# Kernel tuning notes

Measured on AMD Instinct MI355X. Metric: run time of the kernel, lower is better.

## Reference

```python
import jax, jax.numpy as jnp
import numpy as np

B, S, HID = 2, 1024, 4096
H, KV, D = 32, 8, 128
EPS = 1e-6
ROPE_THETA = 1000000.0


def _make_freqs_cis(seq_len, head_dim, theta):
    inv_freq = 1.0 / (theta ** (jnp.arange(0, head_dim, 2, dtype=jnp.float32) / head_dim))
    ang = jnp.arange(seq_len, dtype=jnp.float32)[:, None] * inv_freq[None, :]  # [S, D/2]
    emb = jnp.concatenate([ang, ang], axis=-1)                                 # [S, D]
    cos, sin = jnp.cos(emb), jnp.sin(emb)
    return jnp.stack([cos, sin, -sin], axis=0)                                 # [3, S, D]


def setup_inputs() -> dict:
    key = jax.random.key(0)
    ks = jax.random.split(key, 8)
    scale = 0.02
    return {
        "hidden_states": jax.random.normal(ks[0], (B, S, HID), dtype=jnp.float32),
        "freqs_cis": _make_freqs_cis(S, D, ROPE_THETA),
        "Wq": jax.random.normal(ks[1], (H * D, HID), dtype=jnp.float32) * scale,
        "Wk": jax.random.normal(ks[2], (KV * D, HID), dtype=jnp.float32) * scale,
        "Wv": jax.random.normal(ks[3], (KV * D, HID), dtype=jnp.float32) * scale,
        "Wo": jax.random.normal(ks[4], (HID, H * D), dtype=jnp.float32) * scale,
        "q_norm_w": jnp.ones((D,), jnp.float32) + jax.random.normal(ks[5], (D,), jnp.float32) * scale,
        "k_norm_w": jnp.ones((D,), jnp.float32) + jax.random.normal(ks[6], (D,), jnp.float32) * scale,
    }


def _rmsnorm(x, w):
    # per-head RMSNorm over last dim (rms_norm_add=False -> plain weight multiply)
    return x * jax.lax.rsqrt(jnp.mean(x * x, axis=-1, keepdims=True) + EPS) * w


def _rope(x, cos, sin, nsin):
    # matches apply_rope: e = x*cos; e[:half] += x[half:]*nsin; e[half:] += x[:half]*sin
    half = x.shape[-1] // 2
    e = x * cos
    lo = e[..., :half] + x[..., half:] * nsin[..., :half]
    hi = e[..., half:] + x[..., :half] * sin[..., half:]
    return jnp.concatenate([lo, hi], axis=-1)


def reference(hidden_states, freqs_cis, Wq, Wk, Wv, Wo, q_norm_w, k_norm_w):
    b, s, _ = hidden_states.shape
    # QKV projections (no bias)
    q = jnp.einsum("bsh,oh->bso", hidden_states, Wq).reshape(b, s, H, D).transpose(0, 2, 1, 3)
    k = jnp.einsum("bsh,oh->bso", hidden_states, Wk).reshape(b, s, KV, D).transpose(0, 2, 1, 3)
    v = jnp.einsum("bsh,oh->bso", hidden_states, Wv).reshape(b, s, KV, D).transpose(0, 2, 1, 3)
    # per-head RMSNorm (Qwen3 'gemma3' q/k norms)
    q = _rmsnorm(q, q_norm_w)
    k = _rmsnorm(k, k_norm_w)
    # RoPE
    cos, sin, nsin = freqs_cis[0], freqs_cis[1], freqs_cis[2]  # [S, D] each, broadcast over (b, heads)
    q = _rope(q, cos, sin, nsin)
    k = _rope(k, cos, sin, nsin)
    # GQA: repeat kv heads to match query heads (repeat_interleave dim=1)
    rep = H // KV
    k = jnp.repeat(k, rep, axis=1)
    v = jnp.repeat(v, rep, axis=1)
    # SDPA (no mask, past_key_value=None path)
    scale = D ** -0.5
    attn = jax.nn.softmax(jnp.einsum("bhqd,bhkd->bhqk", q, k) * scale, axis=-1)
    out = jnp.einsum("bhqk,bhkd->bhqd", attn, v)
    out = out.transpose(0, 2, 1, 3).reshape(b, s, H * D)
    return jnp.einsum("bsi,hi->bsh", out, Wo)
```

## Files before the change

### kernel.cpp

```cpp
#include <hip/hip_runtime.h>


typedef __attribute__((ext_vector_type(8))) short s8v;
typedef __attribute__((ext_vector_type(4))) float f4v;
typedef __attribute__((ext_vector_type(8))) unsigned short u8v;
typedef __attribute__((ext_vector_type(4))) float float4v;
typedef __attribute__((ext_vector_type(2))) float float2v;
typedef unsigned short us;

#define SB() __builtin_amdgcn_sched_barrier(0)

__device__ __forceinline__ void BARRIER() {
  asm volatile("" ::: "memory");
  __builtin_amdgcn_s_barrier();
  asm volatile("" ::: "memory");
}

__device__ __forceinline__ us f2b(float f) {
  unsigned u = __builtin_bit_cast(unsigned, f);
  u += 0x7fffu + ((u >> 16) & 1u);
  return (us)(u >> 16);
}
__device__ __forceinline__ float b2f(us h) {
  return __builtin_bit_cast(float, (unsigned)h << 16);
}

__device__ __forceinline__ void gload16(const void* g, void* l) {
  __builtin_amdgcn_global_load_lds(
      (const __attribute__((address_space(1))) unsigned int*)g,
      (__attribute__((address_space(3))) unsigned int*)l, 16, 0, 0);
}

__global__ __launch_bounds__(256) void cvt_all_k(const float* __restrict__ h,
                                                 const float* __restrict__ wq,
                                                 const float* __restrict__ wk,
                                                 const float* __restrict__ wv,
                                                 us* __restrict__ dst) {
  long blk = blockIdx.x;
  const float* src;
  long off;
  if (blk < 4096)        { src = h;  off = 0; }
  else if (blk < 12288)  { src = wq; off = 4096; }
  else if (blk < 14336)  { src = wk; off = 12288; }
  else                   { src = wv; off = 14336; }
  long i = (blk - off) * 2048 + (long)threadIdx.x * 8;
  long o = blk * 2048 + (long)threadIdx.x * 8;
  float4v a = *(const float4v*)(src + i);
  float4v b = *(const float4v*)(src + i + 4);
  u8v v;
  v[0] = f2b(a[0]); v[1] = f2b(a[1]); v[2] = f2b(a[2]); v[3] = f2b(a[3]);
  v[4] = f2b(b[0]); v[5] = f2b(b[1]); v[6] = f2b(b[2]); v[7] = f2b(b[3]);
  *(u8v*)(dst + o) = v;
}

template <int AH, bool F32OUT, bool CVTTAIL>
__global__ __launch_bounds__(512, 2) void gemm8p(const us* __restrict__ A,
                                                 const us* __restrict__ W,
                                                 void* __restrict__ Cv,
                                                 int K, int nkt, int ldc,
                                                 int cm, int cn, int ncn,
                                                 int nGemm,
                                                 const float* __restrict__ csrc,
                                                 us* __restrict__ cdst) {
  if constexpr (CVTTAIL) {
    if ((int)blockIdx.x >= nGemm) {
      long c = (long)((int)blockIdx.x - nGemm) * 512 + threadIdx.x;
      for (; c < 2097152; c += 64 * 512) {
        long i = c * 8;
        float4v x = *(const float4v*)(csrc + i);
        float4v y = *(const float4v*)(csrc + i + 4);
        u8v v;
        v[0] = f2b(x[0]); v[1] = f2b(x[1]); v[2] = f2b(x[2]); v[3] = f2b(x[3]);
        v[4] = f2b(y[0]); v[5] = f2b(y[1]); v[6] = f2b(y[2]); v[7] = f2b(y[3]);
        *(u8v*)(cdst + i) = v;
      }
      return;
    }
  }

  constexpr int FR = AH / 32;
  constexpr int LA = AH / 64;
  constexpr int VM = 2 * LA + 2;

  __shared__ __align__(16) us Ah[2][2][AH * 64];
  __shared__ __align__(16) us Bh[2][2][128 * 64];
  const int tid = threadIdx.x, lane = tid & 63, w = tid >> 6;
  const int wr = w >> 2, wc = w & 3;
  const int lr = lane & 15, lg = lane >> 4;

  const int xcd = (int)blockIdx.x & 7;
  const int i2 = (int)blockIdx.x >> 3;
  const int im = i2 % cm, itn = i2 / cm;
  const long m0 = (long)((xcd / ncn) * cm + im) * (2 * AH);
  const long n0 = (long)((xcd % ncn) * cn + itn) * 256;

  const int rA0 = tid >> 3;
  const int sc0 = ((tid & 7) ^ (rA0 & 7)) << 3;

#define STGH(dst, src, LOADS)                                           \
  do {                                                                  \
    const us* _s = (src);                                               \
    us* _d = (dst);                                                     \
    _Pragma("unroll") for (int l = 0; l < (LOADS); ++l)                 \
      gload16(_s + (long)(rA0 + l * 64) * K + sc0, _d + (l * 512 + tid) * 8); \
  } while (0)

  const us* Asrc = A + m0 * K;
  const us* Bsrc = W + n0 * K;
  const long hKA = (long)AH * K;
  const long hKB = (long)128 * K;

  const int ra = wr * (AH / 2) + lr, rb = wc * 32 + lr;
  const int offA0 = ra * 64 + ((lg ^ (ra & 7)) << 3);
  const int offA1 = ra * 64 + (((4 + lg) ^ (ra & 7)) << 3);
  const int offB0 = rb * 64 + ((lg ^ (rb & 7)) << 3);
  const int offB1 = rb * 64 + (((4 + lg) ^ (rb & 7)) << 3);

  f4v acc[2 * FR][4];
#pragma unroll
  for (int i = 0; i < 2 * FR; ++i)
#pragma unroll
    for (int j = 0; j < 4; ++j) acc[i][j] = (f4v){0.f, 0.f, 0.f, 0.f};

  const int nk = nkt;

  STGH(Ah[0][0], Asrc, LA);
  STGH(Bh[0][0], Bsrc, 2);
  STGH(Bh[0][1], Bsrc + hKB, 2);
  STGH(Ah[0][1], Asrc + hKA, LA);
  STGH(Ah[1][0], Asrc + 64, LA);
  STGH(Bh[1][1], Bsrc + hKB + 64, 2);
  STGH(Ah[1][1], Asrc + hKA + 64, LA);
  asm volatile("s_waitcnt vmcnt(%0)" :: "i"(VM) : "memory");
  BARRIER();

  s8v a[FR][2], b0[2][2], b1[2][2];

#define RD_A(H)                                                         \
  _Pragma("unroll") for (int f = 0; f < FR; ++f) {                      \
    a[f][0] = *(const s8v*)(&Ah[d][H][offA0 + f * 1024]);               \
    a[f][1] = *(const s8v*)(&Ah[d][H][offA1 + f * 1024]);               \
  }
#define RD_B(BB, H)                                                     \
  _Pragma("unroll") for (int g = 0; g < 2; ++g) {                       \
    BB[g][0] = *(const s8v*)(&Bh[d][H][offB0 + g * 1024]);              \
    BB[g][1] = *(const s8v*)(&Bh[d][H][offB1 + g * 1024]);              \
  }
#define QUAD(QM, QN, BB)                                                \
  __builtin_amdgcn_s_setprio(1);                                        \
  _Pragma("unroll") for (int f = 0; f < FR; ++f)                        \
  _Pragma("unroll") for (int g = 0; g < 2; ++g) {                       \
    f4v t = acc[QM * FR + f][QN * 2 + g];                               \
    t = __builtin_amdgcn_mfma_f32_16x16x32_bf16(a[f][0], BB[g][0], t, 0, 0, 0); \
    t = __builtin_amdgcn_mfma_f32_16x16x32_bf16(a[f][1], BB[g][1], t, 0, 0, 0); \
    acc[QM * FR + f][QN * 2 + g] = t;                                   \
  }                                                                     \
  __builtin_amdgcn_s_setprio(0);
#define PREMFMA()                                                       \
  BARRIER();                                                            \
  asm volatile("s_waitcnt lgkmcnt(0)" ::: "memory");                    \
  SB();

  for (int kt = 0; kt < nk; ++kt) {
    const int d = kt & 1;
    const long kb2 = (long)(kt + 2) * 64;
    const bool p1 = (kt + 1 < nk), p2 = (kt + 2 < nk);

    RD_A(0)
    RD_B(b0, 0)
    if (p1) STGH(Bh[d ^ 1][0], Bsrc + (long)(kt + 1) * 64, 2);
    PREMFMA()
    QUAD(0, 0, b0)
    BARRIER();

    RD_B(b1, 1)
    if (p2) STGH(Ah[d][0], Asrc + kb2, LA);
    PREMFMA()
    QUAD(0, 1, b1)
    BARRIER();

    RD_A(1)
    if (p2) STGH(Bh[d][1], Bsrc + hKB + kb2, 2);
    PREMFMA()
    QUAD(1, 1, b1)
    BARRIER();

    if (p2) STGH(Ah[d][1], Asrc + hKA + kb2, LA);
    PREMFMA()
    QUAD(1, 0, b0)
    if (p2) asm volatile("s_waitcnt vmcnt(%0)" :: "i"(VM) : "memory");
    else    asm volatile("s_waitcnt vmcnt(0)" ::: "memory");
    BARRIER();
  }

#pragma unroll
  for (int qm = 0; qm < 2; ++qm)
#pragma unroll
    for (int f = 0; f < FR; ++f) {
      long row = m0 + qm * AH + wr * (AH / 2) + f * 16 + lg * 4;
#pragma unroll
      for (int qn = 0; qn < 2; ++qn)
#pragma unroll
        for (int g = 0; g < 2; ++g) {
          long col = n0 + qn * 128 + wc * 32 + g * 16 + lr;
          f4v v = acc[qm * FR + f][qn * 2 + g];
          if constexpr (F32OUT) {
            float* C = (float*)Cv;
#pragma unroll
            for (int r = 0; r < 4; ++r) C[(row + r) * ldc + col] = v[r];
          } else {
            us* C = (us*)Cv;
#pragma unroll
            for (int r = 0; r < 4; ++r) C[(row + r) * ldc + col] = f2b(v[r]);
          }
        }
    }
#undef STGH
#undef RD_A
#undef RD_B
#undef QUAD
#undef PREMFMA
}

__global__ __launch_bounds__(256, 2) void gemm2p128(const us* __restrict__ A,
                                                    const us* __restrict__ W,
                                                    float* __restrict__ C) {
  constexpr int K = 4096, nk = 64, ldc = 4096;
  __shared__ __align__(16) us Ab[2][128 * 64];
  __shared__ __align__(16) us Bb[2][128 * 64];
  const int tid = threadIdx.x, lane = tid & 63, w = tid >> 6;
  const int wm = w & 1, wn = w >> 1;
  const int lr = lane & 15, lg = lane >> 4;

  const int xcd = (int)blockIdx.x & 7;
  const int i2 = (int)blockIdx.x >> 3;
  const long m0 = (long)(i2 & 15) * 128;
  const long n0 = (long)(xcd * 4 + (i2 >> 4)) * 128;

  const int rA0 = tid >> 3;
  const int sc0 = ((tid & 7) ^ (rA0 & 7)) << 3;

  const us* Asrc = A + m0 * K;
  const us* Bsrc = W + n0 * K;

#define STG1(Sb, buf, src)                                               \
  do {                                                                   \
    const us* _s = (src);                                                \
    _Pragma("unroll") for (int l = 0; l < 4; ++l)                        \
      gload16(_s + (long)(rA0 + l * 32) * K + sc0,                       \
              &Sb[buf][(l * 256 + tid) * 8]);                            \
  } while (0)

  const int ra = wm * 64 + lr;
  const int rb = wn * 64 + lr;
  const int offA0 = ra * 64 + ((lg ^ (ra & 7)) << 3);
  const int offA1 = ra * 64 + (((4 + lg) ^ (ra & 7)) << 3);
  const int offB0 = rb * 64 + ((lg ^ (rb & 7)) << 3);
  const int offB1 = rb * 64 + (((4 + lg) ^ (rb & 7)) << 3);

  f4v acc[4][4];
#pragma unroll
  for (int f = 0; f < 4; ++f)
#pragma unroll
    for (int g = 0; g < 4; ++g) acc[f][g] = (f4v){0.f, 0.f, 0.f, 0.f};

  STG1(Ab, 0, Asrc);
  STG1(Bb, 0, Bsrc);
  STG1(Ab, 1, Asrc + 64);
  asm volatile("s_waitcnt vmcnt(4)" ::: "memory");
  BARRIER();

  for (int kt = 0; kt < nk; ++kt) {
    const int d = kt & 1;
    const bool p1 = (kt + 1 < nk), p2 = (kt + 2 < nk);

    s8v a[4][2], b[4][2];
#pragma unroll
    for (int f = 0; f < 4; ++f) {
      a[f][0] = *(const s8v*)(&Ab[d][offA0 + f * 1024]);
      a[f][1] = *(const s8v*)(&Ab[d][offA1 + f * 1024]);
    }
#pragma unroll
    for (int g = 0; g < 4; ++g) {
      b[g][0] = *(const s8v*)(&Bb[d][offB0 + g * 1024]);
      b[g][1] = *(const s8v*)(&Bb[d][offB1 + g * 1024]);
    }
    if (p1) STG1(Bb, d ^ 1, Bsrc + (long)(kt + 1) * 64);
    asm volatile("s_waitcnt lgkmcnt(0)" ::: "memory");
    BARRIER();
    if (p2) STG1(Ab, d, Asrc + (long)(kt + 2) * 64);

    __builtin_amdgcn_s_setprio(1);
#pragma unroll
    for (int f = 0; f < 4; ++f)
#pragma unroll
      for (int g = 0; g < 4; ++g) {
        f4v t = acc[f][g];
        t = __builtin_amdgcn_mfma_f32_16x16x32_bf16(a[f][0], b[g][0], t, 0, 0, 0);
        t = __builtin_amdgcn_mfma_f32_16x16x32_bf16(a[f][1], b[g][1], t, 0, 0, 0);
        acc[f][g] = t;
      }
    __builtin_amdgcn_s_setprio(0);

    if (p2) asm volatile("s_waitcnt vmcnt(4)" ::: "memory");
    else    asm volatile("s_waitcnt vmcnt(0)" ::: "memory");
    BARRIER();
  }

#pragma unroll
  for (int f = 0; f < 4; ++f) {
    long row = m0 + wm * 64 + f * 16 + lg * 4;
#pragma unroll
    for (int g = 0; g < 4; ++g) {
      long col = n0 + wn * 64 + g * 16 + lr;
      f4v v = acc[f][g];
#pragma unroll
      for (int r = 0; r < 4; ++r) C[(row + r) * ldc + col] = v[r];
    }
  }
#undef STG1
}

__global__ __launch_bounds__(256) void rms_rope_k(us* __restrict__ qkv,
                                                  const float* __restrict__ fc,
                                                  const float* __restrict__ kw) {
  int idx = blockIdx.x * 4 + (threadIdx.x >> 6);
  int lane = threadIdx.x & 63;
  int head = idx & 7;
  int row = idx >> 3;
  int s = row & 1023;
  us* p = qkv + (long)row * 6144 + 4096 + head * 128;

  unsigned v = ((const unsigned*)p)[lane];
  float x0 = b2f((us)(v & 0xffff)), x1 = b2f((us)(v >> 16));
  float ss = x0 * x0 + x1 * x1;
#pragma unroll
  for (int off = 32; off; off >>= 1) ss += __shfl_xor(ss, off);
  float r = rsqrtf(ss * (1.0f / 128.0f) + 1e-6f);
  float2v wv = ((const float2v*)kw)[lane];
  float y0 = x0 * r * wv[0], y1 = x1 * r * wv[1];
  float py0 = __shfl(y0, lane ^ 32);
  float py1 = __shfl(y1, lane ^ 32);
  float2v cv = ((const float2v*)(fc + (long)s * 128))[lane];
  const float* sbase = (lane < 32) ? (fc + 2 * 1024 * 128) : (fc + 1024 * 128);
  float2v sv = ((const float2v*)(sbase + (long)s * 128))[lane];
  float e0 = y0 * cv[0] + py0 * sv[0];
  float e1 = y1 * cv[1] + py1 * sv[1];
  ((unsigned*)p)[lane] = (unsigned)f2b(e0) | ((unsigned)f2b(e1) << 16);
}

__global__ __launch_bounds__(512) void attn_k(const us* __restrict__ qkv,
                                              us* __restrict__ ao,
                                              const float* __restrict__ fc,
                                              const float* __restrict__ qw) {
  __shared__ us Kt[64 * 128];
  __shared__ us Vt[128 * 72];
  __shared__ us Pl[8 * 1024];

  const int bid = blockIdx.x;
  const int qt = bid & 7;
  const int h = (bid >> 3) & 31;
  const int b = bid >> 8;
  const int kvh = h >> 2;
  const int tid = threadIdx.x, lane = tid & 63, w = tid >> 6;
  const int lr = lane & 15, lg = lane >> 4;

  const int srow = qt * 128 + w * 16 + lr;
  const us* Qb = qkv + (long)(b * 1024 + srow) * 6144 + h * 128;
  s8v qr[4];
#pragma unroll
  for (int ks = 0; ks < 4; ++ks) qr[ks] = *(const s8v*)(Qb + ks * 32 + lg * 8);

  float ssq = 0.f;
#pragma unroll
  for (int ks = 0; ks < 4; ++ks)
#pragma unroll
    for (int j = 0; j < 8; ++j) {
      float x = b2f((us)qr[ks][j]);
      ssq += x * x;
    }
  ssq += __shfl_xor(ssq, 16);
  ssq += __shfl_xor(ssq, 32);
  const float rr = rsqrtf(ssq * (1.0f / 128.0f) + 1e-6f);

  const float* cosp = fc + (long)srow * 128;
  const float* sinp = fc + 1024 * 128 + (long)srow * 128;
  s8v qf[4];
#pragma unroll
  for (int ks = 0; ks < 4; ++ks) {
    const int d0 = ks * 32 + lg * 8;
    const int dp = d0 ^ 64;
    const float sgn = (ks < 2) ? -1.f : 1.f;
#pragma unroll
    for (int j = 0; j < 8; ++j) {
      float y  = b2f((us)qr[ks][j])     * rr * qw[d0 + j];
      float yp = b2f((us)qr[ks ^ 2][j]) * rr * qw[dp + j];
      float e = y * cosp[d0 + j] + yp * sgn * sinp[d0 + j];
      qf[ks][j] = (short)f2b(e);
    }
  }

  f4v o[8];
#pragma unroll
  for (int n = 0; n < 8; ++n) o[n] = (f4v){0.f, 0.f, 0.f, 0.f};
  float m[4], l[4];
#pragma unroll
  for (int r = 0; r < 4; ++r) { m[r] = -1e30f; l[r] = 0.f; }

  const float SL = 0.08838834764831845f * 1.4426950408889634f;
  const long krow = (long)b * 1024 * 6144 + 4096 + kvh * 128;
  const long vrow = (long)b * 1024 * 6144 + 5120 + kvh * 128;

  for (int kt = 0; kt < 16; ++kt) {
    __syncthreads();
#pragma unroll
    for (int t = 0; t < 2; ++t) {
      int c = t * 512 + tid;
      int row = c >> 4;
      int sc = (c & 15) ^ (row & 7);
      gload16(qkv + krow + (long)(kt * 64 + row) * 6144 + sc * 8, &Kt[c * 8]);
    }
    {
      int c = tid;
      int kp = c & 31;
      int d0 = (c >> 5) * 8;
      const us* vsrc = qkv + vrow + (long)(kt * 64) * 6144 + d0;
      s8v va = *(const s8v*)(vsrc + (long)(2 * kp) * 6144);
      s8v vb = *(const s8v*)(vsrc + (long)(2 * kp + 1) * 6144);
#pragma unroll
      for (int i = 0; i < 8; ++i) {
        unsigned pk = (unsigned)(us)va[i] | ((unsigned)(us)vb[i] << 16);
        *(unsigned*)&Vt[(d0 + i) * 72 + 2 * kp] = pk;
      }
    }
    __syncthreads();

    f4v sacc[4];
#pragma unroll
    for (int j = 0; j < 4; ++j) sacc[j] = (f4v){0.f, 0.f, 0.f, 0.f};
    __builtin_amdgcn_s_setprio(1);
#pragma unroll
    for (int ks = 0; ks < 4; ++ks) {
#pragma unroll
      for (int j = 0; j < 4; ++j) {
        int key = j * 16 + lr;
        s8v kf = *(const s8v*)&Kt[key * 128 + (((ks * 64 + lg * 16) ^ ((key & 7) << 4)) >> 1)];
        sacc[j] = __builtin_amdgcn_mfma_f32_16x16x32_bf16(qf[ks], kf, sacc[j], 0, 0, 0);
      }
    }
    __builtin_amdgcn_s_setprio(0);

    float sm[4];
#pragma unroll
    for (int r = 0; r < 4; ++r)
      sm[r] = fmaxf(fmaxf(sacc[0][r], sacc[1][r]), fmaxf(sacc[2][r], sacc[3][r]));
#pragma unroll
    for (int off = 1; off < 16; off <<= 1)
#pragma unroll
      for (int r = 0; r < 4; ++r) sm[r] = fmaxf(sm[r], __shfl_xor(sm[r], off));
    bool ok = true;
#pragma unroll
    for (int r = 0; r < 4; ++r) ok = ok && (sm[r] * SL <= m[r] + 8.f);
    if (!__all(ok)) {
#pragma unroll
      for (int r = 0; r < 4; ++r) {
        float nm = fmaxf(m[r], sm[r] * SL);
        float alpha = exp2f(m[r] - nm);
        m[r] = nm;
        l[r] *= alpha;
#pragma unroll
        for (int n = 0; n < 8; ++n) o[n][r] *= alpha;
      }
    }

    us* pw = Pl + w * 1024;
#pragma unroll
    for (int j = 0; j < 4; ++j)
#pragma unroll
      for (int r = 0; r < 4; ++r) {
        float p = exp2f(sacc[j][r] * SL - m[r]);
        l[r] += p;
        int prow = lg * 4 + r, pcol = j * 16 + lr;
        pw[(prow * 128 + ((pcol * 2) ^ ((prow & 7) << 4))) >> 1] = f2b(p);
      }

    __builtin_amdgcn_s_setprio(1);
#pragma unroll
    for (int ks = 0; ks < 2; ++ks) {
      int bo = ks * 64 + lg * 16;
      s8v pf = *(const s8v*)&Pl[w * 1024 + ((lr * 128 + (bo ^ ((lr & 7) << 4))) >> 1)];
#pragma unroll
      for (int n = 0; n < 8; ++n) {
        s8v vf = *(const s8v*)&Vt[(n * 16 + lr) * 72 + ks * 32 + lg * 8];
        o[n] = __builtin_amdgcn_mfma_f32_16x16x32_bf16(pf, vf, o[n], 0, 0, 0);
      }
    }
    __builtin_amdgcn_s_setprio(0);
  }

#pragma unroll
  for (int off = 1; off < 16; off <<= 1)
#pragma unroll
    for (int r = 0; r < 4; ++r) l[r] += __shfl_xor(l[r], off);
  float inv[4];
#pragma unroll
  for (int r = 0; r < 4; ++r) inv[r] = 1.f / l[r];
  const long ob = (long)(b * 1024 + qt * 128 + w * 16) * 4096 + h * 128;
#pragma unroll
  for (int n = 0; n < 8; ++n)
#pragma unroll
    for (int r = 0; r < 4; ++r)
      ao[ob + (long)(lg * 4 + r) * 4096 + n * 16 + lr] = f2b(o[n][r] * inv[r]);
}

extern "C" void kernel_launch(void* const* d_in, const int* in_sizes, int n_in,
                              void* d_out, int out_size, void* d_ws, size_t ws_size,
                              hipStream_t stream) {
  const float* hidden = (const float*)d_in[0];
  const float* fc     = (const float*)d_in[1];
  const float* Wq     = (const float*)d_in[2];
  const float* Wk     = (const float*)d_in[3];
  const float* Wv     = (const float*)d_in[4];
  const float* Wo     = (const float*)d_in[5];
  const float* qw     = (const float*)d_in[6];
  const float* kw     = (const float*)d_in[7];

  us* hb  = (us*)d_ws;
  us* wb  = hb + (long)2048 * 4096;
  us* wbo = wb + (long)6144 * 4096;
  us* qkv = wbo + (long)4096 * 4096;
  us* ao  = qkv + (long)2048 * 6144;

  cvt_all_k<<<16384, 256, 0, stream>>>(hidden, Wq, Wk, Wv, hb);

  gemm8p<128, false, true><<<256, 512, 0, stream>>>(
      hb, wb, qkv, 4096, 64, 6144, 4, 6, 4, 192, Wo, wbo);

  rms_rope_k<<<4096, 256, 0, stream>>>(qkv, fc, kw);

  attn_k<<<512, 512, 0, stream>>>(qkv, ao, fc, qw);

  gemm2p128<<<512, 256, 0, stream>>>(ao, wbo, (float*)d_out);
}
```

Before: 292.3 us.

## Fuse K RMSNorm and RoPE into attention K tile load; tweak GEMM LDS reads

Measured after the change: 336.8 us. +15.2%, slower.

```diff
diff --git a/kernel.cpp b/kernel.cpp
--- a/kernel.cpp
+++ b/kernel.cpp
@@ -169,6 +169,7 @@
     RD_A(0)
     RD_B(b0, 0)
     if (p1) STGH(Bh[d ^ 1][0], Bsrc + (long)(kt + 1) * 64, 2);
+    asm volatile("s_waitcnt lgkmcnt(8)" ::: "memory");
     PREMFMA()
     QUAD(0, 0, b0)
     BARRIER();
@@ -185,6 +186,7 @@
     QUAD(1, 1, b1)
     BARRIER();
 
+    RD_B(b0, 0)
     if (p2) STGH(Ah[d][1], Asrc + hKA + kb2, LA);
     PREMFMA()
     QUAD(1, 0, b0)
@@ -321,38 +323,11 @@
 #undef STG1
 }
 
-__global__ __launch_bounds__(256) void rms_rope_k(us* __restrict__ qkv,
-                                                  const float* __restrict__ fc,
-                                                  const float* __restrict__ kw) {
-  int idx = blockIdx.x * 4 + (threadIdx.x >> 6);
-  int lane = threadIdx.x & 63;
-  int head = idx & 7;
-  int row = idx >> 3;
-  int s = row & 1023;
-  us* p = qkv + (long)row * 6144 + 4096 + head * 128;
-
-  unsigned v = ((const unsigned*)p)[lane];
-  float x0 = b2f((us)(v & 0xffff)), x1 = b2f((us)(v >> 16));
-  float ss = x0 * x0 + x1 * x1;
-#pragma unroll
-  for (int off = 32; off; off >>= 1) ss += __shfl_xor(ss, off);
-  float r = rsqrtf(ss * (1.0f / 128.0f) + 1e-6f);
-  float2v wv = ((const float2v*)kw)[lane];
-  float y0 = x0 * r * wv[0], y1 = x1 * r * wv[1];
-  float py0 = __shfl(y0, lane ^ 32);
-  float py1 = __shfl(y1, lane ^ 32);
-  float2v cv = ((const float2v*)(fc + (long)s * 128))[lane];
-  const float* sbase = (lane < 32) ? (fc + 2 * 1024 * 128) : (fc + 1024 * 128);
-  float2v sv = ((const float2v*)(sbase + (long)s * 128))[lane];
-  float e0 = y0 * cv[0] + py0 * sv[0];
-  float e1 = y1 * cv[1] + py1 * sv[1];
-  ((unsigned*)p)[lane] = (unsigned)f2b(e0) | ((unsigned)f2b(e1) << 16);
-}
-
 __global__ __launch_bounds__(512) void attn_k(const us* __restrict__ qkv,
                                               us* __restrict__ ao,
                                               const float* __restrict__ fc,
-                                              const float* __restrict__ qw) {
+                                              const float* __restrict__ qw,
+                                              const float* __restrict__ kw) {
   __shared__ us Kt[64 * 128];
   __shared__ us Vt[128 * 72];
   __shared__ us Pl[8 * 1024];
@@ -416,9 +391,28 @@
 #pragma unroll
     for (int t = 0; t < 2; ++t) {
       int c = t * 512 + tid;
-      int row = c >> 4;
-      int sc = (c & 15) ^ (row & 7);
-      gload16(qkv + krow + (long)(kt * 64 + row) * 6144 + sc * 8, &Kt[c * 8]);
+      int row = c >> 4, j = c & 15;
+      s8v kr = *(const s8v*)(qkv + krow + (long)(kt * 64 + row) * 6144 + j * 8);
+      float x[8], ssk = 0.f;
+#pragma unroll
+      for (int i = 0; i < 8; ++i) { x[i] = b2f((us)kr[i]); ssk += x[i] * x[i]; }
+#pragma unroll
+      for (int off = 1; off < 16; off <<= 1) ssk += __shfl_xor(ssk, off);
+      float rk = rsqrtf(ssk * (1.0f / 128.0f) + 1e-6f);
+      float y[8];
+#pragma unroll
+      for (int i = 0; i < 8; ++i) y[i] = x[i] * rk * kw[j * 8 + i];
+      int skr = kt * 64 + row;
+      const float* ck = fc + (long)skr * 128 + j * 8;
+      const float* sk = fc + 1024 * 128 + (long)skr * 128 + j * 8;
+      const float sgn = (j < 8) ? -1.f : 1.f;
+      s8v ko;
+#pragma unroll
+      for (int i = 0; i < 8; ++i) {
+        float py = __shfl(y[i], lane ^ 8);
+        ko[i] = (short)f2b(y[i] * ck[i] + py * sgn * sk[i]);
+      }
+      *(s8v*)&Kt[row * 128 + ((j ^ (row & 7)) << 3)] = ko;
     }
     {
       int c = tid;
@@ -536,9 +530,7 @@
   gemm8p<128, false, true><<<256, 512, 0, stream>>>(
       hb, wb, qkv, 4096, 64, 6144, 4, 6, 4, 192, Wo, wbo);
 
-  rms_rope_k<<<4096, 256, 0, stream>>>(qkv, fc, kw);
-
-  attn_k<<<512, 512, 0, stream>>>(qkv, ao, fc, qw);
+  attn_k<<<512, 512, 0, stream>>>(qkv, ao, fc, qw, kw);
 
   gemm2p128<<<512, 256, 0, stream>>>(ao, wbo, (float*)d_out);
 }
```
